# Optimization experiments

Measured on AMD Instinct MI355X. Metric: run time of the kernel, lower is better.

The kernel has to match this reference:

```python
import jax, jax.numpy as jnp
import numpy as np

WINDOW_SIZE = 11
SIGMA = 1.5
C1 = 0.01 ** 2
C2 = 0.03 ** 2
MSE_WEIGHT = 1.0
SSIM_WEIGHT = 0.01


def _gaussian_window(channels):
    # 1D gaussian, normalized, then outer product -> [C,1,K,K] depthwise kernel
    coords = np.arange(WINDOW_SIZE) - WINDOW_SIZE // 2
    g = np.exp(-(coords ** 2) / (2.0 * SIGMA ** 2))
    g = g / g.sum()
    w2d = np.outer(g, g).astype(np.float32)  # [K,K]
    w = np.tile(w2d[None, None], (channels, 1, 1, 1))  # [C,1,K,K]
    return jnp.asarray(w)


def _depthwise_conv(x, w):
    # x: [B,C,H,W], w: [C,1,K,K]; SAME padding, groups=C (matches torch conv2d pad=K//2, groups=C)
    pad = WINDOW_SIZE // 2
    return jax.lax.conv_general_dilated(
        x, w,
        window_strides=(1, 1),
        padding=[(pad, pad), (pad, pad)],
        dimension_numbers=('NCHW', 'OIHW', 'NCHW'),
        feature_group_count=x.shape[1],
    )


def setup_inputs() -> dict:
    key = jax.random.key(0)
    k1, k2 = jax.random.split(key)
    shape = (32, 3, 512, 512)
    predicted = jax.random.uniform(k1, shape, dtype=jnp.float32)
    target = jax.random.uniform(k2, shape, dtype=jnp.float32)
    return {"predicted": predicted, "target": target}


def reference(predicted, target):
    # MSE part
    mse_l = jnp.mean((predicted - target) ** 2)

    # SSIM part (standard pytorch-ssim: gaussian window, size_average=True)
    C = predicted.shape[1]
    w = _gaussian_window(C)

    mu1 = _depthwise_conv(predicted, w)
    mu2 = _depthwise_conv(target, w)
    mu1_sq = mu1 * mu1
    mu2_sq = mu2 * mu2
    mu1_mu2 = mu1 * mu2

    sigma1_sq = _depthwise_conv(predicted * predicted, w) - mu1_sq
    sigma2_sq = _depthwise_conv(target * target, w) - mu2_sq
    sigma12 = _depthwise_conv(predicted * target, w) - mu1_mu2

    ssim_map = ((2.0 * mu1_mu2 + C1) * (2.0 * sigma12 + C2)) / (
        (mu1_sq + mu2_sq + C1) * (sigma1_sq + sigma2_sq + C2)
    )
    ssim_val = jnp.mean(ssim_map)

    return MSE_WEIGHT * mse_l + SSIM_WEIGHT * (1.0 - ssim_val)
```

## Files before the change

### kernel.cpp

```cpp
#include <hip/hip_runtime.h>
#include <hip/hip_fp16.h>


#define WSZ   512
#define TW    64
#define TH    16
#define HALO  5
#define IN_H  (TH + 2*HALO)
#define NPOS  32
#define GX    (WSZ / TW)
#define GY    (WSZ / TH)
#define NSLOT 64
#define SSIM_C1 0.0001f
#define SSIM_C2 0.0009f

#define W0 0.00102838f
#define W1 0.00759876f
#define W2 0.03600080f
#define W3 0.10936080f
#define W4 0.21300560f
#define W5 0.26601170f
__device__ __constant__ const float GW[11] = {W0,W1,W2,W3,W4,W5,W4,W3,W2,W1,W0};

static __device__ __forceinline__ float pkh2(float a, float b) {
    return __builtin_bit_cast(float, __builtin_amdgcn_cvt_pkrtz(a, b));
}

__launch_bounds__(256, 8)
__global__ void fused_mse_ssim(const float* __restrict__ P,
                               const float* __restrict__ T,
                               float* __restrict__ ws) {
    __shared__ float4 sAB[IN_H][NPOS];
    __shared__ float  sC [IN_H][NPOS];
    __shared__ float  red[2][4];

    const int tid = threadIdx.x;
    const int gx0 = blockIdx.x * TW;
    const int gy0 = blockIdx.y * TH;
    const size_t plane = (size_t)blockIdx.z * (WSZ * (size_t)WSZ);
    const float* Pp = P + plane;
    const float* Tp = T + plane;

    float gw[11];
    #pragma unroll
    for (int k = 0; k < 11; ++k) gw[k] = GW[k];

    float mse = 0.f;

    for (int it = tid; it < IN_H * 16; it += 256) {
        const int r = it >> 4;
        const int q = it & 15;
        const int gy = gy0 - HALO + r;
        const int c0 = gx0 + q * 4 - 8;
        const bool rv = ((unsigned)gy < (unsigned)WSZ);
        const float* prow = Pp + (size_t)gy * WSZ;
        const float* trow = Tp + (size_t)gy * WSZ;

        float p[20], t[20];
        #pragma unroll
        for (int b = 0; b < 5; ++b) {
            const int c = c0 + 4 * b;
            float4 pv = make_float4(0.f, 0.f, 0.f, 0.f);
            float4 tv = make_float4(0.f, 0.f, 0.f, 0.f);
            if (rv && ((unsigned)c < (unsigned)WSZ)) {
                pv = *(const float4*)(prow + c);
                tv = *(const float4*)(trow + c);
            }
            p[4*b+0] = pv.x; p[4*b+1] = pv.y; p[4*b+2] = pv.z; p[4*b+3] = pv.w;
            t[4*b+0] = tv.x; t[4*b+1] = tv.y; t[4*b+2] = tv.z; t[4*b+3] = tv.w;
        }

        if ((unsigned)(r - HALO) < (unsigned)TH) {
            #pragma unroll
            for (int i = 0; i < 4; ++i) {
                const float d = p[8 + i] - t[8 + i];
                mse = fmaf(d, d, mse);
            }
        }

        float aP[4]  = {0.f,0.f,0.f,0.f};
        float aT[4]  = {0.f,0.f,0.f,0.f};
        float aPP[4] = {0.f,0.f,0.f,0.f};
        float aTT[4] = {0.f,0.f,0.f,0.f};
        float aPT[4] = {0.f,0.f,0.f,0.f};
        #pragma unroll
        for (int jj = 0; jj < 14; ++jj) {
            const float pv = p[jj + 3];
            const float tv = t[jj + 3];
            const float pp = pv * pv, tt2 = tv * tv, pt = pv * tv;
            #pragma unroll
            for (int o = 0; o < 4; ++o) {
                const int k = jj - o;
                if (k >= 0 && k < 11) {
                    const float w = gw[k];
                    aP[o]  = fmaf(w, pv,  aP[o]);
                    aT[o]  = fmaf(w, tv,  aT[o]);
                    aPP[o] = fmaf(w, pp,  aPP[o]);
                    aTT[o] = fmaf(w, tt2, aTT[o]);
                    aPT[o] = fmaf(w, pt,  aPT[o]);
                }
            }
        }

        sAB[r][2*q]   = make_float4(pkh2(aP[0], aP[1]), pkh2(aT[0], aT[1]),
                                    pkh2(aPP[0],aPP[1]), pkh2(aTT[0],aTT[1]));
        sAB[r][2*q+1] = make_float4(pkh2(aP[2], aP[3]), pkh2(aT[2], aT[3]),
                                    pkh2(aPP[2],aPP[3]), pkh2(aTT[2],aTT[3]));
        sC [r][2*q]   = pkh2(aPT[0], aPT[1]);
        sC [r][2*q+1] = pkh2(aPT[2], aPT[3]);
    }
    __syncthreads();

    __half2 gwh[11];
    #pragma unroll
    for (int k = 0; k < 11; ++k) gwh[k] = __float2half2_rn(gw[k]);

    const int q2 = tid & 31;
    const int y0 = (tid >> 5) * 2;

    __half2 acc[2][5];
    #pragma unroll
    for (int a = 0; a < 2; ++a)
        #pragma unroll
        for (int f = 0; f < 5; ++f)
            acc[a][f] = __float2half2_rn(0.f);

    #pragma unroll
    for (int j = 0; j < 12; ++j) {
        const float4 ab = sAB[y0 + j][q2];
        const float  cc = sC [y0 + j][q2];
        __half2 h[5];
        h[0] = __builtin_bit_cast(__half2, ab.x);
        h[1] = __builtin_bit_cast(__half2, ab.y);
        h[2] = __builtin_bit_cast(__half2, ab.z);
        h[3] = __builtin_bit_cast(__half2, ab.w);
        h[4] = __builtin_bit_cast(__half2, cc);
        if (j < 11) {
            #pragma unroll
            for (int f = 0; f < 5; ++f) acc[0][f] = __hfma2(gwh[j], h[f], acc[0][f]);
        }
        if (j >= 1) {
            #pragma unroll
            for (int f = 0; f < 5; ++f) acc[1][f] = __hfma2(gwh[j-1], h[f], acc[1][f]);
        }
    }

    float ssim = 0.f;
    #pragma unroll
    for (int a = 0; a < 2; ++a) {
        const float2 m1  = __half22float2(acc[a][0]);
        const float2 m2  = __half22float2(acc[a][1]);
        const float2 spp = __half22float2(acc[a][2]);
        const float2 stt = __half22float2(acc[a][3]);
        const float2 spt = __half22float2(acc[a][4]);
        #pragma unroll
        for (int e = 0; e < 2; ++e) {
            const float mu1 = e ? m1.y  : m1.x;
            const float mu2 = e ? m2.y  : m2.x;
            const float vpp = e ? spp.y : spp.x;
            const float vtt = e ? stt.y : stt.x;
            const float vpt = e ? spt.y : spt.x;
            const float mu1sq = mu1 * mu1;
            const float mu2sq = mu2 * mu2;
            const float mu12  = mu1 * mu2;
            const float s1  = vpp - mu1sq;
            const float s2  = vtt - mu2sq;
            const float s12 = vpt - mu12;
            const float num = fmaf(2.f, mu12, SSIM_C1) * fmaf(2.f, s12, SSIM_C2);
            const float den = (mu1sq + mu2sq + SSIM_C1) * (s1 + s2 + SSIM_C2);
            ssim = fmaf(num, __builtin_amdgcn_rcpf(den), ssim);
        }
    }

    #pragma unroll
    for (int off = 32; off > 0; off >>= 1) {
        mse  += __shfl_down(mse, off);
        ssim += __shfl_down(ssim, off);
    }
    const int wid = tid >> 6;
    if ((tid & 63) == 0) { red[0][wid] = mse; red[1][wid] = ssim; }
    __syncthreads();
    if (tid == 0) {
        const float m = red[0][0] + red[0][1] + red[0][2] + red[0][3];
        const float s = red[1][0] + red[1][1] + red[1][2] + red[1][3];
        const int bid  = (blockIdx.z * gridDim.y + blockIdx.y) * gridDim.x + blockIdx.x;
        const int slot = (bid & (NSLOT - 1)) * 16;
        atomicAdd(&ws[slot + 0], m);
        atomicAdd(&ws[slot + 1], s);
    }
}

__global__ void finalize_loss(const float* __restrict__ ws,
                              float* __restrict__ out, float invN) {
    const int t = threadIdx.x;
    float m = ws[t * 16 + 0];
    float s = ws[t * 16 + 1];
    #pragma unroll
    for (int off = 32; off > 0; off >>= 1) {
        m += __shfl_down(m, off);
        s += __shfl_down(s, off);
    }
    if (t == 0) out[0] = m * invN + 0.01f * (1.f - s * invN);
}

extern "C" void kernel_launch(void* const* d_in, const int* in_sizes, int n_in,
                              void* d_out, int out_size, void* d_ws, size_t ws_size,
                              hipStream_t stream) {
    const float* P = (const float*)d_in[0];
    const float* T = (const float*)d_in[1];
    float* out = (float*)d_out;
    float* ws  = (float*)d_ws;

    const int planes = in_sizes[0] / (WSZ * WSZ);
    const float invN = 1.f / (float)in_sizes[0];

    (void)hipMemsetAsync(ws, 0, NSLOT * 16 * sizeof(float), stream);
    dim3 grid(GX, GY, planes);
    fused_mse_ssim<<<grid, 256, 0, stream>>>(P, T, ws);
    finalize_loss<<<1, 64, 0, stream>>>(ws, out, invN);
}
```

Baseline: 264.1 us.

## Compute separable Gaussian convolutions with bf16 MFMA banded-matrix products

```diff
diff --git a/kernel.cpp b/kernel.cpp
--- a/kernel.cpp
+++ b/kernel.cpp
@@ -1,165 +1,165 @@
 #include <hip/hip_runtime.h>
-#include <hip/hip_fp16.h>
 
 
 #define WSZ   512
 #define TW    64
-#define TH    16
-#define HALO  5
-#define IN_H  (TH + 2*HALO)
-#define NPOS  32
-#define GX    (WSZ / TW)
-#define GY    (WSZ / TH)
+#define TH    32
+#define PITCH 48
 #define NSLOT 64
 #define SSIM_C1 0.0001f
 #define SSIM_C2 0.0009f
 
-#define W0 0.00102838f
-#define W1 0.00759876f
-#define W2 0.03600080f
-#define W3 0.10936080f
-#define W4 0.21300560f
-#define W5 0.26601170f
-__device__ __constant__ const float GW[11] = {W0,W1,W2,W3,W4,W5,W4,W3,W2,W1,W0};
-
-static __device__ __forceinline__ float pkh2(float a, float b) {
-    return __builtin_bit_cast(float, __builtin_amdgcn_cvt_pkrtz(a, b));
-}
-
-__launch_bounds__(256, 8)
+__device__ __constant__ float GW[11] = {
+    0.00102838f, 0.00759876f, 0.03600080f, 0.10936080f, 0.21300560f,
+    0.26601170f,
+    0.21300560f, 0.10936080f, 0.03600080f, 0.00759876f, 0.00102838f};
+
+typedef __attribute__((ext_vector_type(8))) short short8;
+typedef __attribute__((ext_vector_type(4))) float f32x4;
+
+static __device__ __forceinline__ unsigned int bf16r(float x) {
+    const unsigned int u = __builtin_bit_cast(unsigned int, x);
+    return (u + 0x7FFFu + ((u >> 16) & 1u)) >> 16;
+}
+static __device__ __forceinline__ unsigned int pkbf(float a, float b) {
+    return bf16r(a) | (bf16r(b) << 16);
+}
+
+static __device__ __forceinline__ short8 mkfrag(const float v[8]) {
+    uint4 u;
+    u.x = pkbf(v[0], v[1]);
+    u.y = pkbf(v[2], v[3]);
+    u.z = pkbf(v[4], v[5]);
+    u.w = pkbf(v[6], v[7]);
+    return __builtin_bit_cast(short8, u);
+}
+
+__launch_bounds__(256, 5)
 __global__ void fused_mse_ssim(const float* __restrict__ P,
                                const float* __restrict__ T,
                                float* __restrict__ ws) {
-    __shared__ float4 sAB[IN_H][NPOS];
-    __shared__ float  sC [IN_H][NPOS];
-    __shared__ float  red[2][4];
-
-    const int tid = threadIdx.x;
-    const int gx0 = blockIdx.x * TW;
-    const int gy0 = blockIdx.y * TH;
+    __shared__ unsigned short sHP[5][64 * PITCH];
+    __shared__ float sEXT[72];
+    __shared__ float red[2][4];
+
+    const int tid  = threadIdx.x;
+    const int wave = tid >> 6;
+    const int lane = tid & 63;
+    const int q    = lane >> 4;
+    const int n15  = lane & 15;
+    const int gx0  = blockIdx.x * TW;
+    const int gy0  = blockIdx.y * TH;
     const size_t plane = (size_t)blockIdx.z * (WSZ * (size_t)WSZ);
     const float* Pp = P + plane;
     const float* Tp = T + plane;
 
-    float gw[11];
-    #pragma unroll
-    for (int k = 0; k < 11; ++k) gw[k] = GW[k];
+    if (tid < 72) {
+        const int i = tid - 32;
+        sEXT[tid] = ((unsigned)i < 11u) ? GW[i] : 0.f;
+    }
 
     float mse = 0.f;
-
-    for (int it = tid; it < IN_H * 16; it += 256) {
-        const int r = it >> 4;
-        const int q = it & 15;
-        const int gy = gy0 - HALO + r;
-        const int c0 = gx0 + q * 4 - 8;
-        const bool rv = ((unsigned)gy < (unsigned)WSZ);
-        const float* prow = Pp + (size_t)gy * WSZ;
-        const float* trow = Tp + (size_t)gy * WSZ;
-
-        float p[20], t[20];
-        #pragma unroll
-        for (int b = 0; b < 5; ++b) {
-            const int c = c0 + 4 * b;
-            float4 pv = make_float4(0.f, 0.f, 0.f, 0.f);
-            float4 tv = make_float4(0.f, 0.f, 0.f, 0.f);
-            if (rv && ((unsigned)c < (unsigned)WSZ)) {
-                pv = *(const float4*)(prow + c);
-                tv = *(const float4*)(trow + c);
-            }
-            p[4*b+0] = pv.x; p[4*b+1] = pv.y; p[4*b+2] = pv.z; p[4*b+3] = pv.w;
-            t[4*b+0] = tv.x; t[4*b+1] = tv.y; t[4*b+2] = tv.z; t[4*b+3] = tv.w;
-        }
-
-        if ((unsigned)(r - HALO) < (unsigned)TH) {
+    {
+        const int r = tid >> 3;
+        const int x = (tid & 7) * 8;
+        const float* pr = Pp + (size_t)(gy0 + r) * WSZ + gx0 + x;
+        const float* tr = Tp + (size_t)(gy0 + r) * WSZ + gx0 + x;
+        #pragma unroll
+        for (int h = 0; h < 2; ++h) {
+            const float4 pv = *(const float4*)(pr + h * 4);
+            const float4 tv = *(const float4*)(tr + h * 4);
+            float d;
+            d = pv.x - tv.x; mse = fmaf(d, d, mse);
+            d = pv.y - tv.y; mse = fmaf(d, d, mse);
+            d = pv.z - tv.z; mse = fmaf(d, d, mse);
+            d = pv.w - tv.w; mse = fmaf(d, d, mse);
+        }
+    }
+    __syncthreads();
+
+    short8 bandH, bandV;
+    {
+        float vh[8], vv[8];
+        const int sH = 29 + q * 8 - n15;
+        const int sV = 32 + q * 8 - n15;
+        #pragma unroll
+        for (int j = 0; j < 8; ++j) { vh[j] = sEXT[sH + j]; vv[j] = sEXT[sV + j]; }
+        bandH = mkfrag(vh);
+        bandV = mkfrag(vv);
+    }
+    const f32x4 zero4 = {0.f, 0.f, 0.f, 0.f};
+
+    #pragma unroll
+    for (int jj = 0; jj < 3; ++jj) {
+        const int job = wave + jj * 4;
+        const int b  = job & 3;
+        const int rb = job >> 2;
+        const int hr   = rb * 16 + n15;
+        const int grow = gy0 - 5 + hr;
+        const bool rowok = ((unsigned)grow < (unsigned)WSZ);
+        const int growc = min(max(grow, 0), WSZ - 1);
+        const int c0 = gx0 - 8 + b * 16 + q * 8;
+        const float* prow = Pp + (size_t)growc * WSZ;
+        const float* trow = Tp + (size_t)growc * WSZ;
+
+        float4 pa = make_float4(0.f,0.f,0.f,0.f), pb = pa, ta = pa, tb = pa;
+        if ((unsigned)c0 < (unsigned)WSZ)       { pa = *(const float4*)(prow + c0);     ta = *(const float4*)(trow + c0); }
+        if ((unsigned)(c0 + 4) < (unsigned)WSZ) { pb = *(const float4*)(prow + c0 + 4); tb = *(const float4*)(trow + c0 + 4); }
+
+        float p[8] = {pa.x, pa.y, pa.z, pa.w, pb.x, pb.y, pb.z, pb.w};
+        float t[8] = {ta.x, ta.y, ta.z, ta.w, tb.x, tb.y, tb.z, tb.w};
+        if (!rowok) {
             #pragma unroll
-            for (int i = 0; i < 4; ++i) {
-                const float d = p[8 + i] - t[8 + i];
-                mse = fmaf(d, d, mse);
-            }
-        }
-
-        float aP[4]  = {0.f,0.f,0.f,0.f};
-        float aT[4]  = {0.f,0.f,0.f,0.f};
-        float aPP[4] = {0.f,0.f,0.f,0.f};
-        float aTT[4] = {0.f,0.f,0.f,0.f};
-        float aPT[4] = {0.f,0.f,0.f,0.f};
-        #pragma unroll
-        for (int jj = 0; jj < 14; ++jj) {
-            const float pv = p[jj + 3];
-            const float tv = t[jj + 3];
-            const float pp = pv * pv, tt2 = tv * tv, pt = pv * tv;
-            #pragma unroll
-            for (int o = 0; o < 4; ++o) {
-                const int k = jj - o;
-                if (k >= 0 && k < 11) {
-                    const float w = gw[k];
-                    aP[o]  = fmaf(w, pv,  aP[o]);
-                    aT[o]  = fmaf(w, tv,  aT[o]);
-                    aPP[o] = fmaf(w, pp,  aPP[o]);
-                    aTT[o] = fmaf(w, tt2, aTT[o]);
-                    aPT[o] = fmaf(w, pt,  aPT[o]);
-                }
-            }
-        }
-
-        sAB[r][2*q]   = make_float4(pkh2(aP[0], aP[1]), pkh2(aT[0], aT[1]),
-                                    pkh2(aPP[0],aPP[1]), pkh2(aTT[0],aTT[1]));
-        sAB[r][2*q+1] = make_float4(pkh2(aP[2], aP[3]), pkh2(aT[2], aT[3]),
-                                    pkh2(aPP[2],aPP[3]), pkh2(aTT[2],aTT[3]));
-        sC [r][2*q]   = pkh2(aPT[0], aPT[1]);
-        sC [r][2*q+1] = pkh2(aPT[2], aPT[3]);
+            for (int i = 0; i < 8; ++i) { p[i] = 0.f; t[i] = 0.f; }
+        }
+        float pp[8], tt[8], pt[8];
+        #pragma unroll
+        for (int i = 0; i < 8; ++i) {
+            pp[i] = p[i] * p[i];
+            tt[i] = t[i] * t[i];
+            pt[i] = p[i] * t[i];
+        }
+        const short8 fP  = mkfrag(p);
+        const short8 fT  = mkfrag(t);
+        const short8 fPP = mkfrag(pp);
+        const short8 fTT = mkfrag(tt);
+        const short8 fPT = mkfrag(pt);
+
+        const f32x4 dP  = __builtin_amdgcn_mfma_f32_16x16x32_bf16(fP,  bandH, zero4, 0, 0, 0);
+        const f32x4 dT  = __builtin_amdgcn_mfma_f32_16x16x32_bf16(fT,  bandH, zero4, 0, 0, 0);
+        const f32x4 dPP = __builtin_amdgcn_mfma_f32_16x16x32_bf16(fPP, bandH, zero4, 0, 0, 0);
+        const f32x4 dTT = __builtin_amdgcn_mfma_f32_16x16x32_bf16(fTT, bandH, zero4, 0, 0, 0);
+        const f32x4 dPT = __builtin_amdgcn_mfma_f32_16x16x32_bf16(fPT, bandH, zero4, 0, 0, 0);
+
+        const int off = (b * 16 + n15) * PITCH + rb * 16 + q * 4;
+        *(uint2*)&sHP[0][off] = make_uint2(pkbf(dP[0],  dP[1]),  pkbf(dP[2],  dP[3]));
+        *(uint2*)&sHP[1][off] = make_uint2(pkbf(dT[0],  dT[1]),  pkbf(dT[2],  dT[3]));
+        *(uint2*)&sHP[2][off] = make_uint2(pkbf(dPP[0], dPP[1]), pkbf(dPP[2], dPP[3]));
+        *(uint2*)&sHP[3][off] = make_uint2(pkbf(dTT[0], dTT[1]), pkbf(dTT[2], dTT[3]));
+        *(uint2*)&sHP[4][off] = make_uint2(pkbf(dPT[0], dPT[1]), pkbf(dPT[2], dPT[3]));
     }
     __syncthreads();
 
-    __half2 gwh[11];
-    #pragma unroll
-    for (int k = 0; k < 11; ++k) gwh[k] = __float2half2_rn(gw[k]);
-
-    const int q2 = tid & 31;
-    const int y0 = (tid >> 5) * 2;
-
-    __half2 acc[2][5];
-    #pragma unroll
-    for (int a = 0; a < 2; ++a)
-        #pragma unroll
-        for (int f = 0; f < 5; ++f)
-            acc[a][f] = __float2half2_rn(0.f);
-
-    #pragma unroll
-    for (int j = 0; j < 12; ++j) {
-        const float4 ab = sAB[y0 + j][q2];
-        const float  cc = sC [y0 + j][q2];
-        __half2 h[5];
-        h[0] = __builtin_bit_cast(__half2, ab.x);
-        h[1] = __builtin_bit_cast(__half2, ab.y);
-        h[2] = __builtin_bit_cast(__half2, ab.z);
-        h[3] = __builtin_bit_cast(__half2, ab.w);
-        h[4] = __builtin_bit_cast(__half2, cc);
-        if (j < 11) {
-            #pragma unroll
-            for (int f = 0; f < 5; ++f) acc[0][f] = __hfma2(gwh[j], h[f], acc[0][f]);
-        }
-        if (j >= 1) {
-            #pragma unroll
-            for (int f = 0; f < 5; ++f) acc[1][f] = __hfma2(gwh[j-1], h[f], acc[1][f]);
-        }
-    }
-
     float ssim = 0.f;
     #pragma unroll
-    for (int a = 0; a < 2; ++a) {
-        const float2 m1  = __half22float2(acc[a][0]);
-        const float2 m2  = __half22float2(acc[a][1]);
-        const float2 spp = __half22float2(acc[a][2]);
-        const float2 stt = __half22float2(acc[a][3]);
-        const float2 spt = __half22float2(acc[a][4]);
-        #pragma unroll
-        for (int e = 0; e < 2; ++e) {
-            const float mu1 = e ? m1.y  : m1.x;
-            const float mu2 = e ? m2.y  : m2.x;
-            const float vpp = e ? spp.y : spp.x;
-            const float vtt = e ? stt.y : stt.x;
-            const float vpt = e ? spt.y : spt.x;
+    for (int jj = 0; jj < 2; ++jj) {
+        const int job = wave + jj * 4;
+        const int yb = job >> 2;
+        const int xb = job & 3;
+        const int off = (xb * 16 + n15) * PITCH + yb * 16 + q * 8;
+        f32x4 d[5];
+        #pragma unroll
+        for (int f = 0; f < 5; ++f) {
+            const short8 bf = *(const short8*)&sHP[f][off];
+            d[f] = __builtin_amdgcn_mfma_f32_16x16x32_bf16(bandV, bf, zero4, 0, 0, 0);
+        }
+        #pragma unroll
+        for (int r = 0; r < 4; ++r) {
+            const float mu1 = d[0][r];
+            const float mu2 = d[1][r];
+            const float vpp = d[2][r];
+            const float vtt = d[3][r];
+            const float vpt = d[4][r];
             const float mu1sq = mu1 * mu1;
             const float mu2sq = mu2 * mu2;
             const float mu12  = mu1 * mu2;
@@ -177,8 +177,7 @@
         mse  += __shfl_down(mse, off);
         ssim += __shfl_down(ssim, off);
     }
-    const int wid = tid >> 6;
-    if ((tid & 63) == 0) { red[0][wid] = mse; red[1][wid] = ssim; }
+    if ((tid & 63) == 0) { red[0][wave] = mse; red[1][wave] = ssim; }
     __syncthreads();
     if (tid == 0) {
         const float m = red[0][0] + red[0][1] + red[0][2] + red[0][3];
@@ -215,7 +214,7 @@
     const float invN = 1.f / (float)in_sizes[0];
 
     (void)hipMemsetAsync(ws, 0, NSLOT * 16 * sizeof(float), stream);
-    dim3 grid(GX, GY, planes);
+    dim3 grid(WSZ / TW, WSZ / TH, planes);
     fused_mse_ssim<<<grid, 256, 0, stream>>>(P, T, ws);
     finalize_loss<<<1, 64, 0, stream>>>(ws, out, invN);
 }
```

New measurement: 270.7 us. 1.02x slower.
